# Optimization experiments

Hardware: AMD Instinct MI355X
Metric: run time of the kernel (lower is better)

Reference implementation:

```python
import jax, jax.numpy as jnp
import numpy as np
import math

E = 1024      # hidden_dim = embed_dim (num_heads=1 so head_dim=E)
ND = 512      # output_dim = asymmetric value dim
N_DOMAIN = 2048
LN_EPS = 1e-5
SCALE = math.sqrt(1.0 / E) * 2.0 * math.log(N_DOMAIN)


def layernorm(x, g, b):
    mu = jnp.mean(x, axis=-1, keepdims=True)
    var = jnp.var(x, axis=-1, keepdims=True)
    return (x - mu) * jax.lax.rsqrt(var + LN_EPS) * g + b


def setup_inputs() -> dict:
    key = jax.random.key(0)
    ks = jax.random.split(key, 5)
    B, L = 8, 2048
    return {
        "x": jax.random.normal(ks[0], (B, L, E), dtype=jnp.float32),
        "in_proj_w": jax.random.normal(ks[1], (2 * E + ND, E), dtype=jnp.float32) * 0.02,
        "w1": jax.random.normal(ks[2], (2048, ND), dtype=jnp.float32) * 0.02,
        "b1": jnp.zeros((2048,), dtype=jnp.float32),
        "w2": jax.random.normal(ks[3], (ND, 2048), dtype=jnp.float32) * 0.02,
        "b2": jnp.zeros((ND,), dtype=jnp.float32),
        "g1": jnp.ones((ND,), dtype=jnp.float32),
        "be1": jnp.zeros((ND,), dtype=jnp.float32),
        "g2": jnp.ones((ND,), dtype=jnp.float32),
        "be2": jnp.zeros((ND,), dtype=jnp.float32),
    }


def reference(x, in_proj_w, w1, b1, w2, b2, g1, be1, g2, be2):
    # fused in-projection (no bias): q,k get E dims, v gets ND dims
    proj = jnp.einsum("ble,fe->blf", x, in_proj_w)
    q = proj[..., :E]
    k = proj[..., E:2 * E]
    v = proj[..., 2 * E:]
    # custom scale: sqrt(1/head_dim) * 2 * log(N)
    scores = jnp.einsum("bld,bsd->bls", q * SCALE, k)  # [B, L, S]
    attn_w = jax.nn.softmax(scores, axis=-1)
    attn_out = jnp.einsum("bls,bsd->bld", attn_w, v)   # [B, L, ND] (no out proj)
    # skip=False (hidden_dim != output_dim): norm1(attn) only
    h = layernorm(attn_out, g1, be1)
    ff = jnp.einsum("bld,fd->blf", h, w1) + b1
    ff = jnp.einsum("blf,df->bld", jax.nn.relu(ff), w2) + b2
    return layernorm(h + ff, g2, be2)
```

## Files before the change

### kernel.cpp

```cpp
#include <hip/hip_runtime.h>
#include <hip/hip_bf16.h>

typedef unsigned short u16;
typedef unsigned int u32;
typedef float f32x4 __attribute__((ext_vector_type(4)));
typedef _Float16 f16x8 __attribute__((ext_vector_type(8)));
typedef u32 u32x4 __attribute__((ext_vector_type(4)));
typedef u32 u32x2 __attribute__((ext_vector_type(2)));

#define SEQ 2048
#define EDIM 1024

__device__ __forceinline__ u16 f2h(float f) {
  _Float16 h = (_Float16)f;
  return __builtin_bit_cast(u16, h);
}
__device__ __forceinline__ float h2f(u16 u) {
  return (float)__builtin_bit_cast(_Float16, u);
}
__device__ __forceinline__ u32 pk(float a, float b) {
  return (u32)f2h(a) | ((u32)f2h(b) << 16);
}

#define N_X  2097152
#define N_WP 327680
#define N_W1 131072
#define N_W2 131072
__global__ __launch_bounds__(256) void cvt_all(const float* __restrict__ x, u16* __restrict__ xb,
                                               const float* __restrict__ wp, u16* __restrict__ wpb,
                                               const float* __restrict__ w1, u16* __restrict__ w1b,
                                               const float* __restrict__ w2, u16* __restrict__ w2b) {
  int i = blockIdx.x * 256 + threadIdx.x;
  const float* src; u16* dst; int li;
  if (i < N_X) { src = x; dst = xb; li = i; }
  else if (i < N_X + N_WP) { src = wp; dst = wpb; li = i - N_X; }
  else if (i < N_X + N_WP + N_W1) { src = w1; dst = w1b; li = i - N_X - N_WP; }
  else if (i < N_X + N_WP + N_W1 + N_W2) { src = w2; dst = w2b; li = i - N_X - N_WP - N_W1; }
  else return;
  const f32x4* p = (const f32x4*)(src + (size_t)li * 8);
  f32x4 a = p[0], b = p[1];
  u32x4 o = {pk(a[0], a[1]), pk(a[2], a[3]), pk(b[0], b[1]), pk(b[2], b[3])};
  *(u32x4*)(dst + (size_t)li * 8) = o;
}

struct GemmP {
  const u16* A; const u16* B;
  int lda, ldb, K;
  long bsA, bsB, bsC;
  int ldc;
  u16* Cb;
  const float* bias;
  const u16* resid;
  u16* qk; u16* vT;
  float scale;
};

template <int EPI>
__global__ __launch_bounds__(256) void gemm_bt(GemmP p) {
  __shared__ __align__(16) char lds[32768];
  const int tid = threadIdx.x;
  const int lane = tid & 63;
  const int wave = tid >> 6;
  const int wm = wave >> 1, wn = wave & 1;
  const int bn0 = blockIdx.x * 128;
  const int bm0 = blockIdx.y * 128;
  const int z = blockIdx.z;

  const u16* gA[4]; const u16* gB[4];
  int ldsA[4], ldsB[4];
  {
    const u16* Ab = p.A + (long)z * p.bsA + (long)bm0 * p.lda;
    const u16* Bb = p.B + (long)z * p.bsB + (long)bn0 * p.ldb;
#pragma unroll
    for (int i = 0; i < 4; ++i) {
      int ch = i * 256 + tid;
      int row = ch >> 3, s = ch & 7;
      int ks = ((s ^ (row & 7)) << 3);
      gA[i] = Ab + (long)row * p.lda + ks;
      gB[i] = Bb + (long)row * p.ldb + ks;
      ldsA[i] = ch * 16;
      ldsB[i] = 16384 + ch * 16;
    }
  }
  auto stage = [&]() {
#pragma unroll
    for (int i = 0; i < 4; ++i) {
      __builtin_amdgcn_global_load_lds(
          (const __attribute__((address_space(1))) u32*)gA[i],
          (__attribute__((address_space(3))) u32*)(lds + ldsA[i]), 16, 0, 0);
      gA[i] += 64;
    }
#pragma unroll
    for (int i = 0; i < 4; ++i) {
      __builtin_amdgcn_global_load_lds(
          (const __attribute__((address_space(1))) u32*)gB[i],
          (__attribute__((address_space(3))) u32*)(lds + ldsB[i]), 16, 0, 0);
      gB[i] += 64;
    }
  };

  int ao[2][4], bo[2][4];
#pragma unroll
  for (int h = 0; h < 2; ++h) {
#pragma unroll
    for (int i = 0; i < 4; ++i) {
      int rA = wm * 64 + i * 16 + (lane & 15);
      ao[h][i] = rA * 128 + ((((h << 2) | (lane >> 4)) ^ (rA & 7)) << 4);
      int rB = wn * 64 + i * 16 + (lane & 15);
      bo[h][i] = 16384 + rB * 128 + ((((h << 2) | (lane >> 4)) ^ (rB & 7)) << 4);
    }
  }

  f32x4 acc[4][4] = {};
  stage();
  const int nk = p.K >> 6;
  for (int kt = 0; kt < nk; ++kt) {
    __syncthreads();
#pragma unroll
    for (int h = 0; h < 2; ++h) {
      f16x8 av[4], bv[4];
#pragma unroll
      for (int i = 0; i < 4; ++i) av[i] = *(const f16x8*)(lds + ao[h][i]);
#pragma unroll
      for (int j = 0; j < 4; ++j) bv[j] = *(const f16x8*)(lds + bo[h][j]);
#pragma unroll
      for (int i = 0; i < 4; ++i)
#pragma unroll
        for (int j = 0; j < 4; ++j)
          acc[i][j] = __builtin_amdgcn_mfma_f32_16x16x32_f16(av[i], bv[j], acc[i][j], 0, 0, 0);
    }
    __syncthreads();
    if (kt + 1 < nk) stage();
  }

#pragma unroll
  for (int i = 0; i < 4; ++i) {
#pragma unroll
    for (int j = 0; j < 4; ++j) {
      int mb = bm0 + wm * 64 + i * 16 + ((lane >> 4) << 2);
      int n = bn0 + wn * 64 + j * 16 + (lane & 15);
      if constexpr (EPI == 1) {
        int b = mb >> 11, l0 = mb & 2047;
        if (n < EDIM) {
          u16* dst = p.qk + (long)b * 4194304 + (long)l0 * 1024 + n;
#pragma unroll
          for (int r = 0; r < 4; ++r) dst[r * 1024] = f2h(acc[i][j][r] * p.scale);
        } else if (n < 2 * EDIM) {
          u16* dst = p.qk + (long)b * 4194304 + 2097152 + (long)l0 * 1024 + (n - EDIM);
#pragma unroll
          for (int r = 0; r < 4; ++r) dst[r * 1024] = f2h(acc[i][j][r]);
        } else {
          u16* dst = p.vT + (long)b * 1048576 + (long)(n - 2 * EDIM) * 2048 + l0;
          u32x2 w = {pk(acc[i][j][0], acc[i][j][1]), pk(acc[i][j][2], acc[i][j][3])};
          *(u32x2*)dst = w;
        }
      } else if constexpr (EPI == 2) {
        u16* dst = p.Cb + (long)mb * p.ldc + n;
        float bias = p.bias[n];
#pragma unroll
        for (int r = 0; r < 4; ++r) dst[(long)r * p.ldc] = f2h(fmaxf(acc[i][j][r] + bias, 0.f));
      } else if constexpr (EPI == 3) {
        float bias = p.bias[n];
        u16* dst = p.Cb + (long)mb * 512 + n;
        const u16* rs = p.resid + (long)mb * 512 + n;
#pragma unroll
        for (int r = 0; r < 4; ++r) dst[r * 512] = f2h(acc[i][j][r] + bias + h2f(rs[r * 512]));
      } else {
        u16* dst = p.Cb + (long)z * p.bsC + (long)mb * p.ldc + n;
#pragma unroll
        for (int r = 0; r < 4; ++r) dst[(long)r * p.ldc] = f2h(acc[i][j][r]);
      }
    }
  }
}

__global__ __launch_bounds__(256) void softmax_rows(const u16* __restrict__ S,
                                                    u16* __restrict__ W, int b0) {
  int r = blockIdx.x;
  int z = r >> 11, l = r & 2047;
  int tid = threadIdx.x, lane = tid & 63, wv = tid >> 6;
  const u16* x = S + (long)r * 2048 + tid * 8;
  u32x4 raw = *(const u32x4*)x;
  float e[8];
#pragma unroll
  for (int q = 0; q < 4; ++q) {
    e[2 * q] = h2f((u16)(raw[q] & 0xffff));
    e[2 * q + 1] = h2f((u16)(raw[q] >> 16));
  }
  float m = e[0];
#pragma unroll
  for (int q = 1; q < 8; ++q) m = fmaxf(m, e[q]);
#pragma unroll
  for (int off = 32; off; off >>= 1) m = fmaxf(m, __shfl_xor(m, off));
  __shared__ float red[8];
  if (lane == 0) red[wv] = m;
  __syncthreads();
  m = fmaxf(fmaxf(red[0], red[1]), fmaxf(red[2], red[3]));
  float s = 0.f;
#pragma unroll
  for (int q = 0; q < 8; ++q) { e[q] = __expf(e[q] - m); s += e[q]; }
#pragma unroll
  for (int off = 32; off; off >>= 1) s += __shfl_xor(s, off);
  if (lane == 0) red[4 + wv] = s;
  __syncthreads();
  s = red[4] + red[5] + red[6] + red[7];
  float inv = 1.f / s;
  u32x4 o = {pk(e[0] * inv, e[1] * inv), pk(e[2] * inv, e[3] * inv),
             pk(e[4] * inv, e[5] * inv), pk(e[6] * inv, e[7] * inv)};
  *(u32x4*)(W + (long)(b0 + z) * 4194304 + (long)l * 2048 + tid * 8) = o;
}

template <int INF16, int OUTF16>
__global__ __launch_bounds__(256) void ln_rows(const void* __restrict__ X,
                                               const float* __restrict__ g,
                                               const float* __restrict__ bb,
                                               void* __restrict__ out) {
  int row = blockIdx.x * 4 + (threadIdx.x >> 6);
  int lane = threadIdx.x & 63;
  float v[8];
  if constexpr (INF16) {
    u32x4 raw = *(const u32x4*)((const u16*)X + (long)row * 512 + lane * 8);
#pragma unroll
    for (int q = 0; q < 4; ++q) {
      v[2 * q] = h2f((u16)(raw[q] & 0xffff));
      v[2 * q + 1] = h2f((u16)(raw[q] >> 16));
    }
  } else {
    const float* x = (const float*)X + (long)row * 512 + lane * 8;
    f32x4 a = *(const f32x4*)x, b = *(const f32x4*)(x + 4);
#pragma unroll
    for (int q = 0; q < 4; ++q) { v[q] = a[q]; v[4 + q] = b[q]; }
  }
  float s = 0.f, sq = 0.f;
#pragma unroll
  for (int q = 0; q < 8; ++q) { s += v[q]; sq += v[q] * v[q]; }
#pragma unroll
  for (int off = 32; off; off >>= 1) {
    s += __shfl_xor(s, off);
    sq += __shfl_xor(sq, off);
  }
  float mean = s * (1.f / 512.f);
  float var = sq * (1.f / 512.f) - mean * mean;
  float rstd = rsqrtf(var + 1e-5f);
  f32x4 g0 = *(const f32x4*)(g + lane * 8), g1v = *(const f32x4*)(g + lane * 8 + 4);
  f32x4 b0 = *(const f32x4*)(bb + lane * 8), b1v = *(const f32x4*)(bb + lane * 8 + 4);
  float o[8];
#pragma unroll
  for (int q = 0; q < 4; ++q) o[q] = (v[q] - mean) * rstd * g0[q] + b0[q];
#pragma unroll
  for (int q = 0; q < 4; ++q) o[4 + q] = (v[4 + q] - mean) * rstd * g1v[q] + b1v[q];
  if constexpr (OUTF16) {
    u32x4 pkd = {pk(o[0], o[1]), pk(o[2], o[3]), pk(o[4], o[5]), pk(o[6], o[7])};
    *(u32x4*)((u16*)out + (long)row * 512 + lane * 8) = pkd;
  } else {
    float* dst = (float*)out + (long)row * 512 + lane * 8;
    *(f32x4*)dst = (f32x4){o[0], o[1], o[2], o[3]};
    *(f32x4*)(dst + 4) = (f32x4){o[4], o[5], o[6], o[7]};
  }
}

extern "C" void kernel_launch(void* const* d_in, const int* in_sizes, int n_in,
                              void* d_out, int out_size, void* d_ws, size_t ws_size,
                              hipStream_t stream) {
  const float* x = (const float*)d_in[0];
  const float* wp = (const float*)d_in[1];
  const float* w1 = (const float*)d_in[2];
  const float* b1 = (const float*)d_in[3];
  const float* w2 = (const float*)d_in[4];
  const float* b2 = (const float*)d_in[5];
  const float* g1 = (const float*)d_in[6];
  const float* be1 = (const float*)d_in[7];
  const float* g2 = (const float*)d_in[8];
  const float* be2 = (const float*)d_in[9];

  char* ws = (char*)d_ws;
  size_t off = 0;
  auto alloc = [&](size_t bytes) {
    char* p = ws + off;
    off += (bytes + 255) & ~(size_t)255;
    return p;
  };
  u16* wpb = (u16*)alloc(2560 * 1024 * 2);
  u16* w1b = (u16*)alloc(2048 * 512 * 2);
  u16* w2b = (u16*)alloc(512 * 2048 * 2);
  char* xb_region = alloc(33554432);
  u16* qk = (u16*)alloc(67108864);
  u16* vT = (u16*)alloc(16777216);
  u16* hb = (u16*)alloc(16777216);
  int bpl = (ws_size >= off + (size_t)67108864) ? 8 : 4;
  char* sc_region = alloc((size_t)bpl * 2048 * 2048 * 2);
  if (off > ws_size) return;

  u16* xb = (u16*)xb_region;
  u16* attn16 = (u16*)xb_region;
  u16* scores = (u16*)sc_region;
  u16* y16 = (u16*)sc_region;
  u16* ff1 = qk;

  const float SC = (float)(0.03125 * 2.0 * 7.6246189861593985);

  cvt_all<<<dim3(10496), dim3(256), 0, stream>>>(x, xb, wp, wpb, w1, w1b, w2, w2b);

  {
    GemmP p{};
    p.A = xb; p.lda = 1024; p.B = wpb; p.ldb = 1024; p.K = 1024;
    p.qk = qk; p.vT = vT; p.scale = SC;
    gemm_bt<1><<<dim3(20, 128, 1), 256, 0, stream>>>(p);
  }

  for (int it = 0; it < 8 / bpl; ++it) {
    int b0 = it * bpl;
    GemmP p{};
    p.A = qk + (long)b0 * 4194304; p.lda = 1024; p.bsA = 4194304;
    p.B = qk + (long)b0 * 4194304 + 2097152; p.ldb = 1024; p.bsB = 4194304;
    p.K = 1024; p.Cb = scores; p.ldc = 2048; p.bsC = 4194304;
    gemm_bt<4><<<dim3(16, 16, bpl), 256, 0, stream>>>(p);
    softmax_rows<<<dim3(bpl * 2048), dim3(256), 0, stream>>>(scores, qk, b0);
  }

  {
    GemmP p{};
    p.A = qk; p.lda = 2048; p.bsA = 4194304;
    p.B = vT; p.ldb = 2048; p.bsB = 1048576;
    p.K = 2048; p.Cb = attn16; p.ldc = 512; p.bsC = 1048576;
    gemm_bt<4><<<dim3(4, 16, 8), 256, 0, stream>>>(p);
  }

  ln_rows<1, 1><<<dim3(4096), dim3(256), 0, stream>>>(attn16, g1, be1, hb);

  {
    GemmP p{};
    p.A = hb; p.lda = 512; p.B = w1b; p.ldb = 512; p.K = 512;
    p.Cb = ff1; p.ldc = 2048; p.bias = b1;
    gemm_bt<2><<<dim3(16, 128, 1), 256, 0, stream>>>(p);
  }

  {
    GemmP p{};
    p.A = ff1; p.lda = 2048; p.B = w2b; p.ldb = 2048; p.K = 2048;
    p.Cb = y16; p.bias = b2; p.resid = hb;
    gemm_bt<3><<<dim3(4, 128, 1), 256, 0, stream>>>(p);
  }

  ln_rows<1, 0><<<dim3(4096), dim3(256), 0, stream>>>(y16, g2, be2, (float*)d_out);
}
```

Baseline: 400.1 us.

## Add 256x256-tile 512-thread GEMM with 4-stage async LDS pipeline for big GEMMs

Adds a new GEMM kernel with 256x256 output tiles, 8 waves, and a 4-deep ring of LDS buffers filled by direct global-to-LDS loads. It double-buffers register fragments and raises wave priority around the MFMA bursts. The kernel is used for the in-projection, the QK^T scores and FFN1 GEMMs, while PV and FFN2 stay on the old kernel. The aim is more operand reuse per tile and better latency hiding, at the cost of 128KB LDS per block, heavy register pressure and fewer blocks in the grid.

```diff
diff --git a/kernel.cpp b/kernel.cpp
--- a/kernel.cpp
+++ b/kernel.cpp
@@ -56,6 +56,148 @@
 };
 
 template <int EPI>
+__global__ __launch_bounds__(512, 2) void gemm256(GemmP p) {
+  __shared__ __align__(16) char lds[131072];
+  const int tid = threadIdx.x;
+  const int lane = tid & 63;
+  const int wave = tid >> 6;
+  const int wm = wave >> 2, wn = wave & 3;
+  const int bn0 = blockIdx.x * 256;
+  const int bm0 = blockIdx.y * 256;
+  const int z = blockIdx.z;
+  const u16* Ab = p.A + (long)z * p.bsA + (long)bm0 * p.lda;
+  const u16* Bb = p.B + (long)z * p.bsB + (long)bn0 * p.ldb;
+
+  const int ch0 = tid, ch1 = tid + 512;
+  const int r0 = ch0 >> 2, s0 = ch0 & 3;
+  const int r1 = ch1 >> 2, s1 = ch1 & 3;
+  const long srcA0 = (long)r0 * p.lda + ((s0 ^ ((r0 >> 1) & 3)) << 3);
+  const long srcA1 = (long)r1 * p.lda + ((s1 ^ ((r1 >> 1) & 3)) << 3);
+  const long srcB0 = (long)r0 * p.ldb + ((s0 ^ ((r0 >> 1) & 3)) << 3);
+  const long srcB1 = (long)r1 * p.ldb + ((s1 ^ ((r1 >> 1) & 3)) << 3);
+
+  auto stage = [&](int s) {
+    const int base = (s & 3) * 32768;
+    const int k0 = s * 32;
+    __builtin_amdgcn_global_load_lds(
+        (const __attribute__((address_space(1))) u32*)(Ab + k0 + srcA0),
+        (__attribute__((address_space(3))) u32*)(lds + base + ch0 * 16), 16, 0, 0);
+    __builtin_amdgcn_global_load_lds(
+        (const __attribute__((address_space(1))) u32*)(Ab + k0 + srcA1),
+        (__attribute__((address_space(3))) u32*)(lds + base + ch1 * 16), 16, 0, 0);
+    __builtin_amdgcn_global_load_lds(
+        (const __attribute__((address_space(1))) u32*)(Bb + k0 + srcB0),
+        (__attribute__((address_space(3))) u32*)(lds + base + 16384 + ch0 * 16), 16, 0, 0);
+    __builtin_amdgcn_global_load_lds(
+        (const __attribute__((address_space(1))) u32*)(Bb + k0 + srcB1),
+        (__attribute__((address_space(3))) u32*)(lds + base + 16384 + ch1 * 16), 16, 0, 0);
+  };
+
+  int aoff[8], boff[4];
+#pragma unroll
+  for (int m = 0; m < 8; ++m) {
+    int r = wm * 128 + m * 16 + (lane & 15);
+    aoff[m] = r * 64 + ((((lane >> 4)) ^ ((r >> 1) & 3)) << 4);
+  }
+#pragma unroll
+  for (int n = 0; n < 4; ++n) {
+    int r = wn * 64 + n * 16 + (lane & 15);
+    boff[n] = 16384 + r * 64 + ((((lane >> 4)) ^ ((r >> 1) & 3)) << 4);
+  }
+
+  f32x4 acc[8][4] = {};
+  f16x8 avc[8], bvc[4], avn[8], bvn[4];
+
+  stage(0); stage(1); stage(2);
+  asm volatile("s_waitcnt vmcnt(8)" ::: "memory");
+  __builtin_amdgcn_s_barrier();
+  {
+    const char* b0 = lds;
+#pragma unroll
+    for (int m = 0; m < 8; ++m) avc[m] = *(const f16x8*)(b0 + aoff[m]);
+#pragma unroll
+    for (int n = 0; n < 4; ++n) bvc[n] = *(const f16x8*)(b0 + boff[n]);
+  }
+
+  const int NS = p.K >> 5;
+  for (int s = 0; s < NS; s += 2) {
+    asm volatile("s_waitcnt vmcnt(4)" ::: "memory");
+    __builtin_amdgcn_s_barrier();
+    {
+      const char* bn = lds + ((s + 1) & 3) * 32768;
+#pragma unroll
+      for (int m = 0; m < 8; ++m) avn[m] = *(const f16x8*)(bn + aoff[m]);
+#pragma unroll
+      for (int n = 0; n < 4; ++n) bvn[n] = *(const f16x8*)(bn + boff[n]);
+      if (s + 3 < NS) stage(s + 3);
+    }
+    __builtin_amdgcn_sched_barrier(0);
+    __builtin_amdgcn_s_setprio(1);
+#pragma unroll
+    for (int m = 0; m < 8; ++m)
+#pragma unroll
+      for (int n = 0; n < 4; ++n)
+        acc[m][n] = __builtin_amdgcn_mfma_f32_16x16x32_f16(avc[m], bvc[n], acc[m][n], 0, 0, 0);
+    __builtin_amdgcn_s_setprio(0);
+
+    asm volatile("s_waitcnt vmcnt(4)" ::: "memory");
+    __builtin_amdgcn_s_barrier();
+    {
+      if (s + 2 < NS) {
+        const char* bn2 = lds + ((s + 2) & 3) * 32768;
+#pragma unroll
+        for (int m = 0; m < 8; ++m) avc[m] = *(const f16x8*)(bn2 + aoff[m]);
+#pragma unroll
+        for (int n = 0; n < 4; ++n) bvc[n] = *(const f16x8*)(bn2 + boff[n]);
+      }
+      if (s + 4 < NS) stage(s + 4);
+    }
+    __builtin_amdgcn_sched_barrier(0);
+    __builtin_amdgcn_s_setprio(1);
+#pragma unroll
+    for (int m = 0; m < 8; ++m)
+#pragma unroll
+      for (int n = 0; n < 4; ++n)
+        acc[m][n] = __builtin_amdgcn_mfma_f32_16x16x32_f16(avn[m], bvn[n], acc[m][n], 0, 0, 0);
+    __builtin_amdgcn_s_setprio(0);
+  }
+
+#pragma unroll
+  for (int i = 0; i < 8; ++i) {
+#pragma unroll
+    for (int j = 0; j < 4; ++j) {
+      int mb = bm0 + wm * 128 + i * 16 + ((lane >> 4) << 2);
+      int n = bn0 + wn * 64 + j * 16 + (lane & 15);
+      if constexpr (EPI == 1) {
+        int b = mb >> 11, l0 = mb & 2047;
+        if (n < EDIM) {
+          u16* dst = p.qk + (long)b * 4194304 + (long)l0 * 1024 + n;
+#pragma unroll
+          for (int r = 0; r < 4; ++r) dst[r * 1024] = f2h(acc[i][j][r] * p.scale);
+        } else if (n < 2 * EDIM) {
+          u16* dst = p.qk + (long)b * 4194304 + 2097152 + (long)l0 * 1024 + (n - EDIM);
+#pragma unroll
+          for (int r = 0; r < 4; ++r) dst[r * 1024] = f2h(acc[i][j][r]);
+        } else {
+          u16* dst = p.vT + (long)b * 1048576 + (long)(n - 2 * EDIM) * 2048 + l0;
+          u32x2 w = {pk(acc[i][j][0], acc[i][j][1]), pk(acc[i][j][2], acc[i][j][3])};
+          *(u32x2*)dst = w;
+        }
+      } else if constexpr (EPI == 2) {
+        u16* dst = p.Cb + (long)mb * p.ldc + n;
+        float bias = p.bias[n];
+#pragma unroll
+        for (int r = 0; r < 4; ++r) dst[(long)r * p.ldc] = f2h(fmaxf(acc[i][j][r] + bias, 0.f));
+      } else {
+        u16* dst = p.Cb + (long)z * p.bsC + (long)mb * p.ldc + n;
+#pragma unroll
+        for (int r = 0; r < 4; ++r) dst[(long)r * p.ldc] = f2h(acc[i][j][r]);
+      }
+    }
+  }
+}
+
+template <int EPI>
 __global__ __launch_bounds__(256) void gemm_bt(GemmP p) {
   __shared__ __align__(16) char lds[32768];
   const int tid = threadIdx.x;
@@ -139,27 +281,7 @@
     for (int j = 0; j < 4; ++j) {
       int mb = bm0 + wm * 64 + i * 16 + ((lane >> 4) << 2);
       int n = bn0 + wn * 64 + j * 16 + (lane & 15);
-      if constexpr (EPI == 1) {
-        int b = mb >> 11, l0 = mb & 2047;
-        if (n < EDIM) {
-          u16* dst = p.qk + (long)b * 4194304 + (long)l0 * 1024 + n;
-#pragma unroll
-          for (int r = 0; r < 4; ++r) dst[r * 1024] = f2h(acc[i][j][r] * p.scale);
-        } else if (n < 2 * EDIM) {
-          u16* dst = p.qk + (long)b * 4194304 + 2097152 + (long)l0 * 1024 + (n - EDIM);
-#pragma unroll
-          for (int r = 0; r < 4; ++r) dst[r * 1024] = f2h(acc[i][j][r]);
-        } else {
-          u16* dst = p.vT + (long)b * 1048576 + (long)(n - 2 * EDIM) * 2048 + l0;
-          u32x2 w = {pk(acc[i][j][0], acc[i][j][1]), pk(acc[i][j][2], acc[i][j][3])};
-          *(u32x2*)dst = w;
-        }
-      } else if constexpr (EPI == 2) {
-        u16* dst = p.Cb + (long)mb * p.ldc + n;
-        float bias = p.bias[n];
-#pragma unroll
-        for (int r = 0; r < 4; ++r) dst[(long)r * p.ldc] = f2h(fmaxf(acc[i][j][r] + bias, 0.f));
-      } else if constexpr (EPI == 3) {
+      if constexpr (EPI == 3) {
         float bias = p.bias[n];
         u16* dst = p.Cb + (long)mb * 512 + n;
         const u16* rs = p.resid + (long)mb * 512 + n;
@@ -305,7 +427,7 @@
     GemmP p{};
     p.A = xb; p.lda = 1024; p.B = wpb; p.ldb = 1024; p.K = 1024;
     p.qk = qk; p.vT = vT; p.scale = SC;
-    gemm_bt<1><<<dim3(20, 128, 1), 256, 0, stream>>>(p);
+    gemm256<1><<<dim3(10, 64, 1), 512, 0, stream>>>(p);
   }
 
   for (int it = 0; it < 8 / bpl; ++it) {
@@ -314,7 +436,7 @@
     p.A = qk + (long)b0 * 4194304; p.lda = 1024; p.bsA = 4194304;
     p.B = qk + (long)b0 * 4194304 + 2097152; p.ldb = 1024; p.bsB = 4194304;
     p.K = 1024; p.Cb = scores; p.ldc = 2048; p.bsC = 4194304;
-    gemm_bt<4><<<dim3(16, 16, bpl), 256, 0, stream>>>(p);
+    gemm256<4><<<dim3(8, 8, bpl), 512, 0, stream>>>(p);
     softmax_rows<<<dim3(bpl * 2048), dim3(256), 0, stream>>>(scores, qk, b0);
   }
 
@@ -332,7 +454,7 @@
     GemmP p{};
     p.A = hb; p.lda = 512; p.B = w1b; p.ldb = 512; p.K = 512;
     p.Cb = ff1; p.ldc = 2048; p.bias = b1;
-    gemm_bt<2><<<dim3(16, 128, 1), 256, 0, stream>>>(p);
+    gemm256<2><<<dim3(8, 64, 1), 512, 0, stream>>>(p);
   }
 
   {
```

Result: no change. 394.6 us (-1.4%).

## Double-buffer LDS staging and switch GEMM to 32x32x16 MFMA tiles

Applied to the files above, without the earlier changes.

The GEMM kernel now keeps two LDS buffers, so the next K-tile is loaded asynchronously while the current one is consumed, and one of the two barriers per iteration is dropped. Each wave's 64x64 output tile is now computed with four 32x32x16 MFMAs per k-step instead of sixteen 16x16x32 ones, which cuts LDS fragment reads per MFMA. The epilogue is rewritten for the 32x32 accumulator layout. LDS use doubles to 64KB per block, which may lower occupancy. The global_load_lds into the other buffer is issued without an explicit vmcnt wait before the next barrier, which is a possible race.

```diff
diff --git a/kernel.cpp b/kernel.cpp
--- a/kernel.cpp
+++ b/kernel.cpp
@@ -4,6 +4,7 @@
 typedef unsigned short u16;
 typedef unsigned int u32;
 typedef float f32x4 __attribute__((ext_vector_type(4)));
+typedef float f32x16 __attribute__((ext_vector_type(16)));
 typedef _Float16 f16x8 __attribute__((ext_vector_type(8)));
 typedef u32 u32x4 __attribute__((ext_vector_type(4)));
 typedef u32 u32x2 __attribute__((ext_vector_type(2)));
@@ -57,7 +58,7 @@
 
 template <int EPI>
 __global__ __launch_bounds__(256) void gemm_bt(GemmP p) {
-  __shared__ __align__(16) char lds[32768];
+  __shared__ __align__(16) char lds[65536];
   const int tid = threadIdx.x;
   const int lane = tid & 63;
   const int wave = tid >> 6;
@@ -82,93 +83,103 @@
       ldsB[i] = 16384 + ch * 16;
     }
   }
-  auto stage = [&]() {
+  auto stage = [&](int buf) {
+    char* dst = lds + buf * 32768;
 #pragma unroll
     for (int i = 0; i < 4; ++i) {
       __builtin_amdgcn_global_load_lds(
           (const __attribute__((address_space(1))) u32*)gA[i],
-          (__attribute__((address_space(3))) u32*)(lds + ldsA[i]), 16, 0, 0);
+          (__attribute__((address_space(3))) u32*)(dst + ldsA[i]), 16, 0, 0);
       gA[i] += 64;
     }
 #pragma unroll
     for (int i = 0; i < 4; ++i) {
       __builtin_amdgcn_global_load_lds(
           (const __attribute__((address_space(1))) u32*)gB[i],
-          (__attribute__((address_space(3))) u32*)(lds + ldsB[i]), 16, 0, 0);
+          (__attribute__((address_space(3))) u32*)(dst + ldsB[i]), 16, 0, 0);
       gB[i] += 64;
     }
   };
 
-  int ao[2][4], bo[2][4];
-#pragma unroll
-  for (int h = 0; h < 2; ++h) {
-#pragma unroll
-    for (int i = 0; i < 4; ++i) {
-      int rA = wm * 64 + i * 16 + (lane & 15);
-      ao[h][i] = rA * 128 + ((((h << 2) | (lane >> 4)) ^ (rA & 7)) << 4);
-      int rB = wn * 64 + i * 16 + (lane & 15);
-      bo[h][i] = 16384 + rB * 128 + ((((h << 2) | (lane >> 4)) ^ (rB & 7)) << 4);
-    }
-  }
-
-  f32x4 acc[4][4] = {};
-  stage();
+  int aoff[2][4], boff[2][4];
+#pragma unroll
+  for (int i = 0; i < 2; ++i) {
+    int rA = wm * 64 + i * 32 + (lane & 31);
+    int rB = wn * 64 + i * 32 + (lane & 31);
+#pragma unroll
+    for (int ks = 0; ks < 4; ++ks) {
+      aoff[i][ks] = rA * 128 + ((((ks << 1) | (lane >> 5)) ^ (rA & 7)) << 4);
+      boff[i][ks] = 16384 + rB * 128 + ((((ks << 1) | (lane >> 5)) ^ (rB & 7)) << 4);
+    }
+  }
+
+  f32x16 acc[2][2] = {};
+  stage(0);
   const int nk = p.K >> 6;
+  int cur = 0;
   for (int kt = 0; kt < nk; ++kt) {
     __syncthreads();
-#pragma unroll
-    for (int h = 0; h < 2; ++h) {
-      f16x8 av[4], bv[4];
-#pragma unroll
-      for (int i = 0; i < 4; ++i) av[i] = *(const f16x8*)(lds + ao[h][i]);
-#pragma unroll
-      for (int j = 0; j < 4; ++j) bv[j] = *(const f16x8*)(lds + bo[h][j]);
-#pragma unroll
-      for (int i = 0; i < 4; ++i)
-#pragma unroll
-        for (int j = 0; j < 4; ++j)
-          acc[i][j] = __builtin_amdgcn_mfma_f32_16x16x32_f16(av[i], bv[j], acc[i][j], 0, 0, 0);
-    }
-    __syncthreads();
-    if (kt + 1 < nk) stage();
-  }
-
-#pragma unroll
-  for (int i = 0; i < 4; ++i) {
-#pragma unroll
-    for (int j = 0; j < 4; ++j) {
-      int mb = bm0 + wm * 64 + i * 16 + ((lane >> 4) << 2);
-      int n = bn0 + wn * 64 + j * 16 + (lane & 15);
-      if constexpr (EPI == 1) {
-        int b = mb >> 11, l0 = mb & 2047;
-        if (n < EDIM) {
-          u16* dst = p.qk + (long)b * 4194304 + (long)l0 * 1024 + n;
-#pragma unroll
-          for (int r = 0; r < 4; ++r) dst[r * 1024] = f2h(acc[i][j][r] * p.scale);
-        } else if (n < 2 * EDIM) {
-          u16* dst = p.qk + (long)b * 4194304 + 2097152 + (long)l0 * 1024 + (n - EDIM);
-#pragma unroll
-          for (int r = 0; r < 4; ++r) dst[r * 1024] = f2h(acc[i][j][r]);
+    if (kt + 1 < nk) stage(cur ^ 1);
+    const char* base = lds + cur * 32768;
+#pragma unroll
+    for (int ks = 0; ks < 4; ++ks) {
+      f16x8 a0 = *(const f16x8*)(base + aoff[0][ks]);
+      f16x8 a1 = *(const f16x8*)(base + aoff[1][ks]);
+      f16x8 b0 = *(const f16x8*)(base + boff[0][ks]);
+      f16x8 b1 = *(const f16x8*)(base + boff[1][ks]);
+      acc[0][0] = __builtin_amdgcn_mfma_f32_32x32x16_f16(a0, b0, acc[0][0], 0, 0, 0);
+      acc[0][1] = __builtin_amdgcn_mfma_f32_32x32x16_f16(a0, b1, acc[0][1], 0, 0, 0);
+      acc[1][0] = __builtin_amdgcn_mfma_f32_32x32x16_f16(a1, b0, acc[1][0], 0, 0, 0);
+      acc[1][1] = __builtin_amdgcn_mfma_f32_32x32x16_f16(a1, b1, acc[1][1], 0, 0, 0);
+    }
+    cur ^= 1;
+  }
+
+#pragma unroll
+  for (int i = 0; i < 2; ++i) {
+#pragma unroll
+    for (int j = 0; j < 2; ++j) {
+      int nn = bn0 + wn * 64 + j * 32 + (lane & 31);
+#pragma unroll
+      for (int rq = 0; rq < 4; ++rq) {
+        int mrow = bm0 + wm * 64 + i * 32 + rq * 8 + ((lane >> 5) << 2);
+        float v0 = acc[i][j][rq * 4 + 0], v1 = acc[i][j][rq * 4 + 1];
+        float v2 = acc[i][j][rq * 4 + 2], v3 = acc[i][j][rq * 4 + 3];
+        if constexpr (EPI == 1) {
+          int b = mrow >> 11, l0 = mrow & 2047;
+          if (nn < EDIM) {
+            u16* dst = p.qk + (long)b * 4194304 + (long)l0 * 1024 + nn;
+            dst[0] = f2h(v0 * p.scale); dst[1024] = f2h(v1 * p.scale);
+            dst[2048] = f2h(v2 * p.scale); dst[3072] = f2h(v3 * p.scale);
+          } else if (nn < 2 * EDIM) {
+            u16* dst = p.qk + (long)b * 4194304 + 2097152 + (long)l0 * 1024 + (nn - EDIM);
+            dst[0] = f2h(v0); dst[1024] = f2h(v1);
+            dst[2048] = f2h(v2); dst[3072] = f2h(v3);
+          } else {
+            u16* dst = p.vT + (long)b * 1048576 + (long)(nn - 2 * EDIM) * 2048 + l0;
+            u32x2 w = {pk(v0, v1), pk(v2, v3)};
+            *(u32x2*)dst = w;
+          }
+        } else if constexpr (EPI == 2) {
+          float bias = p.bias[nn];
+          u16* dst = p.Cb + (long)mrow * p.ldc + nn;
+          dst[0] = f2h(fmaxf(v0 + bias, 0.f));
+          dst[p.ldc] = f2h(fmaxf(v1 + bias, 0.f));
+          dst[2 * p.ldc] = f2h(fmaxf(v2 + bias, 0.f));
+          dst[3 * p.ldc] = f2h(fmaxf(v3 + bias, 0.f));
+        } else if constexpr (EPI == 3) {
+          float bias = p.bias[nn];
+          u16* dst = p.Cb + (long)mrow * 512 + nn;
+          const u16* rs = p.resid + (long)mrow * 512 + nn;
+          dst[0] = f2h(v0 + bias + h2f(rs[0]));
+          dst[512] = f2h(v1 + bias + h2f(rs[512]));
+          dst[1024] = f2h(v2 + bias + h2f(rs[1024]));
+          dst[1536] = f2h(v3 + bias + h2f(rs[1536]));
         } else {
-          u16* dst = p.vT + (long)b * 1048576 + (long)(n - 2 * EDIM) * 2048 + l0;
-          u32x2 w = {pk(acc[i][j][0], acc[i][j][1]), pk(acc[i][j][2], acc[i][j][3])};
-          *(u32x2*)dst = w;
+          u16* dst = p.Cb + (long)z * p.bsC + (long)mrow * p.ldc + nn;
+          dst[0] = f2h(v0); dst[p.ldc] = f2h(v1);
+          dst[2 * p.ldc] = f2h(v2); dst[3 * p.ldc] = f2h(v3);
         }
-      } else if constexpr (EPI == 2) {
-        u16* dst = p.Cb + (long)mb * p.ldc + n;
-        float bias = p.bias[n];
-#pragma unroll
-        for (int r = 0; r < 4; ++r) dst[(long)r * p.ldc] = f2h(fmaxf(acc[i][j][r] + bias, 0.f));
-      } else if constexpr (EPI == 3) {
-        float bias = p.bias[n];
-        u16* dst = p.Cb + (long)mb * 512 + n;
-        const u16* rs = p.resid + (long)mb * 512 + n;
-#pragma unroll
-        for (int r = 0; r < 4; ++r) dst[r * 512] = f2h(acc[i][j][r] + bias + h2f(rs[r * 512]));
-      } else {
-        u16* dst = p.Cb + (long)z * p.bsC + (long)mb * p.ldc + n;
-#pragma unroll
-        for (int r = 0; r < 4; ++r) dst[(long)r * p.ldc] = f2h(acc[i][j][r]);
       }
     }
   }
```

Measured after the change: 403.9 us. About the same (+0.9%).
